# Performance work log

Measured on AMD Instinct MI355X. Metric: run time of the kernel, lower is better.

## Reference

```python
import jax, jax.numpy as jnp
import numpy as np

IGNORE_INDEX = -100
BETA = 0.1
VOCAB = 32000
HIDDEN = 4096
TWO_B = 8   # concatenated [chosen; rejected]
SEQ = 512


def setup_inputs() -> dict:
    key = jax.random.key(0)
    k1, k2, k3, k4, k5 = jax.random.split(key, 5)
    lin_weight = jax.random.normal(k1, (VOCAB, HIDDEN), dtype=jnp.float32) * 0.02
    _input = jax.random.normal(k2, (TWO_B, SEQ, HIDDEN), dtype=jnp.float32)
    target = jax.random.randint(k3, (TWO_B, SEQ), 0, VOCAB, dtype=jnp.int64)
    ref_chosen_logps = jax.random.normal(k4, (TWO_B // 2,), dtype=jnp.float32)
    ref_rejected_logps = jax.random.normal(k5, (TWO_B // 2,), dtype=jnp.float32)
    bias = jnp.zeros((VOCAB,), dtype=jnp.float32)
    return {"lin_weight": lin_weight, "_input": _input, "target": target,
            "ref_chosen_logps": ref_chosen_logps, "ref_rejected_logps": ref_rejected_logps,
            "bias": bias}


def reference(lin_weight, _input, target, ref_chosen_logps, ref_rejected_logps, bias):
    B2 = target.shape[0]
    len_chosen = B2 // 2
    # fused linear + log-softmax (materialized here; the kernel chunks this)
    logits = jnp.einsum("bth,vh->btv", _input, lin_weight) + bias  # [2B, T, V]
    logp = jax.nn.log_softmax(logits, axis=-1)
    mask = (target != IGNORE_INDEX)
    safe_tgt = jnp.where(mask, target, 0)
    per_tok = jnp.take_along_axis(logp, safe_tgt[..., None], axis=-1)[..., 0]
    per_tok = jnp.where(mask, per_tok, 0.0)                         # [2B, T]
    cnt = mask.sum(axis=-1).astype(per_tok.dtype)                   # tokens per sequence
    avg_logps = per_tok.sum(axis=-1) / cnt                          # average logp per sequence
    chosen_logps = avg_logps[:len_chosen]
    rejected_logps = avg_logps[len_chosen:]
    # NLL loss on chosen half, normalized by chosen non-ignored token count
    nll_loss = -per_tok[:len_chosen].sum() / mask[:len_chosen].sum().astype(per_tok.dtype)
    # DPO preference loss
    chosen_adv = chosen_logps - ref_chosen_logps
    rejected_adv = rejected_logps - ref_rejected_logps
    pref_logits = BETA * (chosen_adv - rejected_adv)
    pref_loss = -jnp.mean(jax.nn.log_sigmoid(pref_logits))
    return pref_loss + nll_loss
```

## Files before the change

### kernel.cpp

```cpp
#include <hip/hip_runtime.h>
#include <hip/hip_bf16.h>
#include <stdint.h>

#define M_TOK 4096
#define NV    32000
#define KH    4096
#define BM    128
#define BN    128
#define BK    64
#define NBLK  (NV / BN)
#define MBLK  (M_TOK / BM)
#define IGNORE_INDEX (-100)

typedef __bf16 bf16;
typedef bf16  bf16x8 __attribute__((ext_vector_type(8)));
typedef bf16  bf16x4 __attribute__((ext_vector_type(4)));
typedef float f32x4  __attribute__((ext_vector_type(4)));

__device__ __forceinline__ void async_copy16(const void* g, void* l) {
    __builtin_amdgcn_global_load_lds(
        (const __attribute__((address_space(1))) void*)g,
        (__attribute__((address_space(3))) void*)l, 16, 0, 0);
}

__global__ __launch_bounds__(256) void cvt_bf16_kernel(const float* __restrict__ src,
                                                       bf16* __restrict__ dst, int n4) {
    int i = blockIdx.x * blockDim.x + threadIdx.x;
    int stride = gridDim.x * blockDim.x;
    const float4* s4 = (const float4*)src;
    bf16x4* d4 = (bf16x4*)dst;
    for (; i < n4; i += stride) {
        float4 v = s4[i];
        bf16x4 o;
        o[0] = (bf16)v.x; o[1] = (bf16)v.y; o[2] = (bf16)v.z; o[3] = (bf16)v.w;
        d4[i] = o;
    }
}

__global__ __launch_bounds__(256) void tlogit_kernel(const float* __restrict__ inp,
                                                     const float* __restrict__ W,
                                                     const float* __restrict__ bias,
                                                     const int* __restrict__ target,
                                                     float* __restrict__ tlogit) {
    const int wave = threadIdx.x >> 6, lane = threadIdx.x & 63;
    const int t = blockIdx.x * 4 + wave;
    if (t >= M_TOK) return;
    int tg = target[t];
    int row = (tg == IGNORE_INDEX) ? 0 : tg;
    const float4* a4 = (const float4*)(inp + (long)t * KH);
    const float4* w4 = (const float4*)(W + (long)row * KH);
    float acc = 0.f;
#pragma unroll
    for (int i = 0; i < 16; i++) {
        float4 a = a4[i * 64 + lane];
        float4 w = w4[i * 64 + lane];
        acc += a.x * w.x + a.y * w.y + a.z * w.z + a.w * w.w;
    }
#pragma unroll
    for (int d = 1; d < 64; d <<= 1) acc += __shfl_xor(acc, d, 64);
    if (lane == 0) tlogit[t] = acc + bias[row];
}

template<bool PRECONV>
__global__ __launch_bounds__(256) void gemm_lse_kernel(const bf16* __restrict__ A,
                                                       const void* __restrict__ Wv,
                                                       const float* __restrict__ bias,
                                                       float* __restrict__ pm,
                                                       float* __restrict__ ps) {
    const int tid = threadIdx.x;
    const int wave = tid >> 6, lane = tid & 63;
    const int wm = wave & 1, wn = wave >> 1;
    const int bx = blockIdx.x;
    const int mblk = bx & 31;
    const int nblk = bx >> 5;
    const int m0 = mblk * BM, n0 = nblk * BN;

    __shared__ bf16 sA[BM * BK];
    __shared__ bf16 sB[BN * BK];
    __shared__ float red_m[2][BM];
    __shared__ float red_s[2][BM];

    f32x4 acc[4][4] = {};

    const int srow  = tid >> 3;
    const int slot  = tid & 7;
    const int chunk = slot ^ (srow & 7);
    const bf16* aptr = A + (long)(m0 + srow) * KH + chunk * 8;
    bf16* sA_dst = sA + tid * 8;
    bf16* sB_dst = sB + tid * 8;

    const bf16*  Wb = (const bf16*)Wv;
    const float* Wf = (const float*)Wv;
    const bf16*  bptr16 = Wb + (long)(n0 + srow) * KH + chunk * 8;
    const float* bptr32 = Wf + (long)(n0 + srow) * KH + chunk * 8;

    for (int k0 = 0; k0 < KH; k0 += BK) {
#pragma unroll
        for (int i = 0; i < 4; i++)
            async_copy16(aptr + (long)i * 32 * KH + k0, sA_dst + i * 2048);
        if (PRECONV) {
#pragma unroll
            for (int i = 0; i < 4; i++)
                async_copy16(bptr16 + (long)i * 32 * KH + k0, sB_dst + i * 2048);
        } else {
#pragma unroll
            for (int i = 0; i < 4; i++) {
                const float* wp = bptr32 + (long)i * 32 * KH + k0;
                float4 w0 = *(const float4*)(wp);
                float4 w1 = *(const float4*)(wp + 4);
                bf16x8 b;
                b[0] = (bf16)w0.x; b[1] = (bf16)w0.y; b[2] = (bf16)w0.z; b[3] = (bf16)w0.w;
                b[4] = (bf16)w1.x; b[5] = (bf16)w1.y; b[6] = (bf16)w1.z; b[7] = (bf16)w1.w;
                *(bf16x8*)(sB + (i * 32 + srow) * BK + slot * 8) = b;
            }
        }
        __syncthreads();
#pragma unroll
        for (int kk = 0; kk < BK; kk += 32) {
            bf16x8 af[4], bfr[4];
            const int rbase = wm * 64 + (lane & 15);
            const int cbase = wn * 64 + (lane & 15);
            const int c = (kk >> 3) + (lane >> 4);
            const int xoff = ((c ^ (lane & 7)) << 3);
#pragma unroll
            for (int t = 0; t < 4; t++)
                af[t] = *(const bf16x8*)(sA + (rbase + t * 16) * BK + xoff);
#pragma unroll
            for (int t = 0; t < 4; t++)
                bfr[t] = *(const bf16x8*)(sB + (cbase + t * 16) * BK + xoff);
#pragma unroll
            for (int mt = 0; mt < 4; mt++)
#pragma unroll
                for (int nt = 0; nt < 4; nt++)
                    acc[mt][nt] = __builtin_amdgcn_mfma_f32_16x16x32_bf16(
                        af[mt], bfr[nt], acc[mt][nt], 0, 0, 0);
        }
        __syncthreads();
    }

    float bv[4];
#pragma unroll
    for (int nt = 0; nt < 4; nt++)
        bv[nt] = bias[n0 + wn * 64 + nt * 16 + (lane & 15)];

#pragma unroll
    for (int mt = 0; mt < 4; mt++) {
        float rm[4], rs[4];
#pragma unroll
        for (int r = 0; r < 4; r++) {
            float v0 = acc[mt][0][r] + bv[0];
            float v1 = acc[mt][1][r] + bv[1];
            float v2 = acc[mt][2][r] + bv[2];
            float v3 = acc[mt][3][r] + bv[3];
            float mx = fmaxf(fmaxf(v0, v1), fmaxf(v2, v3));
#pragma unroll
            for (int d = 1; d < 16; d <<= 1) mx = fmaxf(mx, __shfl_xor(mx, d, 64));
            float s = __expf(v0 - mx) + __expf(v1 - mx) + __expf(v2 - mx) + __expf(v3 - mx);
#pragma unroll
            for (int d = 1; d < 16; d <<= 1) s += __shfl_xor(s, d, 64);
            rm[r] = mx; rs[r] = s;
        }
        if ((lane & 15) == 0) {
            int rl = wm * 64 + mt * 16 + (lane >> 4) * 4;
#pragma unroll
            for (int r = 0; r < 4; r++) {
                red_m[wn][rl + r] = rm[r];
                red_s[wn][rl + r] = rs[r];
            }
        }
    }
    __syncthreads();
    if (tid < BM) {
        float m0v = red_m[0][tid], s0v = red_s[0][tid];
        float m1v = red_m[1][tid], s1v = red_s[1][tid];
        float mm = fmaxf(m0v, m1v);
        float ss = s0v * __expf(m0v - mm) + s1v * __expf(m1v - mm);
        long idx = (long)nblk * M_TOK + m0 + tid;
        pm[idx] = mm;
        ps[idx] = ss;
    }
}

__global__ __launch_bounds__(256) void lse_combine_kernel(const float* __restrict__ pm,
                                                          const float* __restrict__ ps,
                                                          const float* __restrict__ tlogit,
                                                          const int* __restrict__ target,
                                                          float* __restrict__ per_tok) {
    int t = blockIdx.x * blockDim.x + threadIdx.x;
    if (t >= M_TOK) return;
    float m = -1e30f, s = 0.f;
    for (int j = 0; j < NBLK; j++) {
        float mj = pm[j * M_TOK + t];
        float sj = ps[j * M_TOK + t];
        if (mj > m) {
            s = s * expf(m - mj) + sj;
            m = mj;
        } else {
            s += sj * expf(mj - m);
        }
    }
    float lse = m + logf(s);
    int tg = target[t];
    per_tok[t] = (tg != IGNORE_INDEX) ? (tlogit[t] - lse) : 0.0f;
}

__global__ __launch_bounds__(512) void final_kernel(const float* __restrict__ per_tok,
                                                    const int* __restrict__ target,
                                                    const float* __restrict__ refc,
                                                    const float* __restrict__ refr,
                                                    float* __restrict__ out) {
    __shared__ float ssum[8];
    __shared__ float scnt[8];
    const int w = threadIdx.x >> 6, lane = threadIdx.x & 63;
    float sum = 0.f, cnt = 0.f;
#pragma unroll
    for (int i = 0; i < 8; i++) {
        int t = w * 512 + i * 64 + lane;
        sum += per_tok[t];
        cnt += (target[t] != IGNORE_INDEX) ? 1.f : 0.f;
    }
#pragma unroll
    for (int d = 1; d < 64; d <<= 1) {
        sum += __shfl_xor(sum, d, 64);
        cnt += __shfl_xor(cnt, d, 64);
    }
    if (lane == 0) { ssum[w] = sum; scnt[w] = cnt; }
    __syncthreads();
    if (threadIdx.x == 0) {
        float avg[8];
#pragma unroll
        for (int i = 0; i < 8; i++) avg[i] = ssum[i] / scnt[i];
        float nll_num = 0.f, nll_den = 0.f;
#pragma unroll
        for (int i = 0; i < 4; i++) { nll_num += ssum[i]; nll_den += scnt[i]; }
        float nll = -nll_num / nll_den;
        float pref = 0.f;
#pragma unroll
        for (int i = 0; i < 4; i++) {
            float x = 0.1f * ((avg[i] - refc[i]) - (avg[i + 4] - refr[i]));
            float ls = (x >= 0.f) ? -log1pf(expf(-x)) : (x - log1pf(expf(x)));
            pref += -ls;
        }
        pref *= 0.25f;
        out[0] = pref + nll;
    }
}

extern "C" void kernel_launch(void* const* d_in, const int* in_sizes, int n_in,
                              void* d_out, int out_size, void* d_ws, size_t ws_size,
                              hipStream_t stream) {
    const float* W    = (const float*)d_in[0];
    const float* inp  = (const float*)d_in[1];
    const int*   tgt  = (const int*)d_in[2];
    const float* refc = (const float*)d_in[3];
    const float* refr = (const float*)d_in[4];
    const float* bias = (const float*)d_in[5];
    float* out = (float*)d_out;

    char* ws = (char*)d_ws;
    size_t off = 0;
    bf16* A16 = (bf16*)(ws + off); off += (size_t)M_TOK * KH * sizeof(bf16);
    float* pm = (float*)(ws + off); off += (size_t)NBLK * M_TOK * sizeof(float);
    float* ps = (float*)(ws + off); off += (size_t)NBLK * M_TOK * sizeof(float);
    float* tl = (float*)(ws + off); off += (size_t)M_TOK * sizeof(float);
    float* ptk = (float*)(ws + off); off += (size_t)M_TOK * sizeof(float);
    bf16* W16 = (bf16*)(ws + off);
    size_t need = off + (size_t)NV * KH * sizeof(bf16);

    cvt_bf16_kernel<<<4096, 256, 0, stream>>>(inp, A16, (M_TOK * KH) / 4);
    tlogit_kernel<<<M_TOK / 4, 256, 0, stream>>>(inp, W, bias, tgt, tl);
    if (ws_size >= need) {
        cvt_bf16_kernel<<<16384, 256, 0, stream>>>(W, W16, (int)(((size_t)NV * KH) / 4));
        gemm_lse_kernel<true><<<MBLK * NBLK, 256, 0, stream>>>(A16, (const void*)W16, bias, pm, ps);
    } else {
        gemm_lse_kernel<false><<<MBLK * NBLK, 256, 0, stream>>>(A16, (const void*)W, bias, pm, ps);
    }
    lse_combine_kernel<<<(M_TOK + 255) / 256, 256, 0, stream>>>(pm, ps, tl, tgt, ptk);
    final_kernel<<<1, 512, 0, stream>>>(ptk, tgt, refc, refr, out);
}
```

Baseline: 2.127 ms.

## Add 256x256-tile double-buffered bf16 MFMA GEMM with fused log-sum-exp partials

Replaces the 128x128 GEMM+LSE kernel with a 512-thread, 256x256-tile kernel for the pre-converted-weight path. The new kernel double-buffers 128KB of LDS through async global-to-LDS copies into XOR-swizzled tiles. It interleaves quarter-tile MFMA groups with the next tile's loads, using explicit barriers, waitcnts and setprio. Blocks are remapped so neighbouring tiles land on the same XCD, and the combine kernel now takes the column-block count as a parameter. The aim is more data reuse per LDS byte and better overlap of loads with MFMA work. The cost is very high register and LDS use, so only one block fits per CU, and the hand-tuned wait counts are fragile.

Result: faster. 1.714 ms (-19.4%).

```diff
diff --git a/kernel.cpp b/kernel.cpp
--- a/kernel.cpp
+++ b/kernel.cpp
@@ -5,12 +5,14 @@
 #define M_TOK 4096
 #define NV    32000
 #define KH    4096
+#define KTILES 64
+#define IGNORE_INDEX (-100)
+
 #define BM    128
 #define BN    128
 #define BK    64
-#define NBLK  (NV / BN)
-#define MBLK  (M_TOK / BM)
-#define IGNORE_INDEX (-100)
+#define NBLK_OLD  (NV / BN)
+#define MBLK_OLD  (M_TOK / BM)
 
 typedef __bf16 bf16;
 typedef bf16  bf16x8 __attribute__((ext_vector_type(8)));
@@ -61,6 +63,180 @@
     if (lane == 0) tlogit[t] = acc + bias[row];
 }
 
+__global__ __launch_bounds__(512, 2) void gemm_lse256_kernel(
+    const bf16* __restrict__ A, const bf16* __restrict__ W16,
+    const float* __restrict__ bias, float* __restrict__ pm, float* __restrict__ ps)
+{
+    __shared__ __align__(16) char smem[131072];
+    const int tid = threadIdx.x;
+    const int lane = tid & 63;
+    const int wid = tid >> 6;
+    const int wm = wid >> 2, wn = wid & 3;
+
+    const int bx = blockIdx.x;
+    const int wg = (bx & 7) * 250 + (bx >> 3);
+    const int nblk = wg >> 4;
+    const int mblk = wg & 15;
+    const int m0 = mblk << 8;
+    const int n0 = nblk << 8;
+
+    const int srow = tid >> 3, slot = tid & 7;
+    const int chunk = slot ^ (srow & 7);
+    const bf16* aSrc = A   + (size_t)(m0 + srow) * KH + chunk * 8;
+    const bf16* bSrc = W16 + (size_t)(n0 + srow) * KH + chunk * 8;
+    char* dA0 = smem +      0 + tid * 16;
+    char* dB0 = smem +  32768 + tid * 16;
+    char* dA1 = smem +  65536 + tid * 16;
+    char* dB1 = smem +  98304 + tid * 16;
+
+#define STG_A(DST, h, tt) do { if ((tt) < KTILES) {                            \
+        const bf16* _s = aSrc + (size_t)(h) * 128 * KH + (size_t)(tt) * 64;    \
+        async_copy16(_s,                   (DST) + (h) * 16384);               \
+        async_copy16(_s + (size_t)64 * KH, (DST) + (h) * 16384 + 8192); } } while (0)
+#define STG_B(DST, h, tt) do { if ((tt) < KTILES) {                            \
+        const bf16* _s = bSrc + (size_t)(h) * 128 * KH + (size_t)(tt) * 64;    \
+        async_copy16(_s,                   (DST) + (h) * 16384);               \
+        async_copy16(_s + (size_t)64 * KH, (DST) + (h) * 16384 + 8192); } } while (0)
+
+    const int rA = wm * 128 + (lane & 15);
+    const int rB = wn * 64  + (lane & 15);
+    const int co0 = ((((lane >> 4) + 0) ^ (lane & 7)) << 3);
+    const int co1 = ((((lane >> 4) + 4) ^ (lane & 7)) << 3);
+
+    const bf16* sA[2] = { (const bf16*)(smem),         (const bf16*)(smem + 65536) };
+    const bf16* sB[2] = { (const bf16*)(smem + 32768), (const bf16*)(smem + 98304) };
+
+    f32x4 acc[8][4] = {};
+    bf16x8 regA[8], regB0[4], regB1[4];
+
+#define MFMA_Q(MB, NB, BR)                                                      \
+    _Pragma("unroll")                                                           \
+    for (int mt = 0; mt < 4; ++mt)                                              \
+        _Pragma("unroll")                                                       \
+        for (int nt = 0; nt < 2; ++nt)                                          \
+            _Pragma("unroll")                                                   \
+            for (int ks = 0; ks < 2; ++ks)                                      \
+                acc[(MB) + mt][(NB) + nt] = __builtin_amdgcn_mfma_f32_16x16x32_bf16( \
+                    regA[mt * 2 + ks], BR[nt * 2 + ks], acc[(MB) + mt][(NB) + nt], 0, 0, 0);
+
+#define TILE_BODY(b, t, DA_O, DB_C, DA_C) do {                                  \
+                                                      \
+    _Pragma("unroll") for (int mt = 0; mt < 4; ++mt) {                          \
+        regA[mt * 2]     = *(const bf16x8*)(sA[b] + (rA + mt * 16) * 64 + co0); \
+        regA[mt * 2 + 1] = *(const bf16x8*)(sA[b] + (rA + mt * 16) * 64 + co1); } \
+    _Pragma("unroll") for (int nt = 0; nt < 2; ++nt) {                          \
+        regB0[nt * 2]     = *(const bf16x8*)(sB[b] + (rB + nt * 16) * 64 + co0); \
+        regB0[nt * 2 + 1] = *(const bf16x8*)(sB[b] + (rB + nt * 16) * 64 + co1); } \
+    STG_A(DA_O, 1, (t) + 1);                                                    \
+    __builtin_amdgcn_s_barrier();                                               \
+    asm volatile("s_waitcnt lgkmcnt(0)" ::: "memory");                          \
+    __builtin_amdgcn_sched_barrier(0);                                          \
+    __builtin_amdgcn_s_setprio(1);                                              \
+    MFMA_Q(0, 0, regB0)                                                         \
+    __builtin_amdgcn_s_setprio(0);                                              \
+    __builtin_amdgcn_s_barrier();                                               \
+                                                      \
+    _Pragma("unroll") for (int nt = 0; nt < 2; ++nt) {                          \
+        regB1[nt * 2]     = *(const bf16x8*)(sB[b] + (rB + (nt + 2) * 16) * 64 + co0); \
+        regB1[nt * 2 + 1] = *(const bf16x8*)(sB[b] + (rB + (nt + 2) * 16) * 64 + co1); } \
+    __builtin_amdgcn_s_barrier();                                               \
+    asm volatile("s_waitcnt lgkmcnt(0)" ::: "memory");                          \
+    __builtin_amdgcn_sched_barrier(0);                                          \
+    __builtin_amdgcn_s_setprio(1);                                              \
+    MFMA_Q(0, 2, regB1)                                                         \
+    __builtin_amdgcn_s_setprio(0);                                              \
+    __builtin_amdgcn_s_barrier();                                               \
+                                                      \
+    _Pragma("unroll") for (int mt = 0; mt < 4; ++mt) {                          \
+        regA[mt * 2]     = *(const bf16x8*)(sA[b] + (rA + (mt + 4) * 16) * 64 + co0); \
+        regA[mt * 2 + 1] = *(const bf16x8*)(sA[b] + (rA + (mt + 4) * 16) * 64 + co1); } \
+    STG_B(DB_C, 0, (t) + 2);                                                    \
+    __builtin_amdgcn_s_barrier();                                               \
+    asm volatile("s_waitcnt lgkmcnt(0)" ::: "memory");                          \
+    __builtin_amdgcn_sched_barrier(0);                                          \
+    __builtin_amdgcn_s_setprio(1);                                              \
+    MFMA_Q(4, 2, regB1)                                                         \
+    __builtin_amdgcn_s_setprio(0);                                              \
+    __builtin_amdgcn_s_barrier();                                               \
+                                                      \
+    STG_B(DB_C, 1, (t) + 2);                                                    \
+    STG_A(DA_C, 0, (t) + 2);                                                    \
+    __builtin_amdgcn_s_barrier();                                               \
+    __builtin_amdgcn_s_setprio(1);                                              \
+    MFMA_Q(4, 0, regB0)                                                         \
+    __builtin_amdgcn_s_setprio(0);                                              \
+    if ((t) + 2 < KTILES) { asm volatile("s_waitcnt vmcnt(6)" ::: "memory"); }  \
+    else                  { asm volatile("s_waitcnt vmcnt(0)" ::: "memory"); }  \
+    __builtin_amdgcn_s_barrier();                                               \
+} while (0)
+
+    STG_A(dA0, 0, 0); STG_A(dA0, 1, 0);
+    STG_B(dB0, 0, 0); STG_B(dB0, 1, 0);
+    STG_B(dB1, 0, 1); STG_B(dB1, 1, 1);
+    STG_A(dA1, 0, 1);
+    asm volatile("s_waitcnt vmcnt(6)" ::: "memory");
+    __builtin_amdgcn_s_barrier();
+
+#pragma unroll 1
+    for (int t = 0; t < KTILES; t += 2) {
+        TILE_BODY(0, t,     dA1, dB0, dA0);
+        TILE_BODY(1, t + 1, dA0, dB1, dA1);
+    }
+
+    float bv[4];
+#pragma unroll
+    for (int nt = 0; nt < 4; ++nt)
+        bv[nt] = bias[n0 + wn * 64 + nt * 16 + (lane & 15)];
+
+    float (*red_m)[256] = (float (*)[256])(smem);
+    float (*red_s)[256] = (float (*)[256])(smem + 4096);
+
+#pragma unroll
+    for (int mt = 0; mt < 8; ++mt) {
+        float rm[4], rs[4];
+#pragma unroll
+        for (int r = 0; r < 4; ++r) {
+            float v0 = acc[mt][0][r] + bv[0];
+            float v1 = acc[mt][1][r] + bv[1];
+            float v2 = acc[mt][2][r] + bv[2];
+            float v3 = acc[mt][3][r] + bv[3];
+            float mx = fmaxf(fmaxf(v0, v1), fmaxf(v2, v3));
+#pragma unroll
+            for (int d = 1; d < 16; d <<= 1) mx = fmaxf(mx, __shfl_xor(mx, d, 64));
+            float s = __expf(v0 - mx) + __expf(v1 - mx) + __expf(v2 - mx) + __expf(v3 - mx);
+#pragma unroll
+            for (int d = 1; d < 16; d <<= 1) s += __shfl_xor(s, d, 64);
+            rm[r] = mx; rs[r] = s;
+        }
+        if ((lane & 15) == 0) {
+            int rl = wm * 128 + mt * 16 + (lane >> 4) * 4;
+#pragma unroll
+            for (int r = 0; r < 4; ++r) {
+                red_m[wn][rl + r] = rm[r];
+                red_s[wn][rl + r] = rs[r];
+            }
+        }
+    }
+    __syncthreads();
+    if (tid < 256) {
+        float mm = red_m[0][tid], ss = red_s[0][tid];
+#pragma unroll
+        for (int j = 1; j < 4; ++j) {
+            float mj = red_m[j][tid], sj = red_s[j][tid];
+            float m2 = fmaxf(mm, mj);
+            ss = ss * __expf(mm - m2) + sj * __expf(mj - m2);
+            mm = m2;
+        }
+        size_t idx = (size_t)nblk * M_TOK + m0 + tid;
+        pm[idx] = mm;
+        ps[idx] = ss;
+    }
+#undef TILE_BODY
+#undef MFMA_Q
+#undef STG_A
+#undef STG_B
+}
+
 template<bool PRECONV>
 __global__ __launch_bounds__(256) void gemm_lse_kernel(const bf16* __restrict__ A,
                                                        const void* __restrict__ Wv,
@@ -185,11 +361,12 @@
                                                           const float* __restrict__ ps,
                                                           const float* __restrict__ tlogit,
                                                           const int* __restrict__ target,
-                                                          float* __restrict__ per_tok) {
+                                                          float* __restrict__ per_tok,
+                                                          int nblkN) {
     int t = blockIdx.x * blockDim.x + threadIdx.x;
     if (t >= M_TOK) return;
     float m = -1e30f, s = 0.f;
-    for (int j = 0; j < NBLK; j++) {
+    for (int j = 0; j < nblkN; j++) {
         float mj = pm[j * M_TOK + t];
         float sj = ps[j * M_TOK + t];
         if (mj > m) {
@@ -260,8 +437,8 @@
     char* ws = (char*)d_ws;
     size_t off = 0;
     bf16* A16 = (bf16*)(ws + off); off += (size_t)M_TOK * KH * sizeof(bf16);
-    float* pm = (float*)(ws + off); off += (size_t)NBLK * M_TOK * sizeof(float);
-    float* ps = (float*)(ws + off); off += (size_t)NBLK * M_TOK * sizeof(float);
+    float* pm = (float*)(ws + off); off += (size_t)NBLK_OLD * M_TOK * sizeof(float);
+    float* ps = (float*)(ws + off); off += (size_t)NBLK_OLD * M_TOK * sizeof(float);
     float* tl = (float*)(ws + off); off += (size_t)M_TOK * sizeof(float);
     float* ptk = (float*)(ws + off); off += (size_t)M_TOK * sizeof(float);
     bf16* W16 = (bf16*)(ws + off);
@@ -271,10 +448,11 @@
     tlogit_kernel<<<M_TOK / 4, 256, 0, stream>>>(inp, W, bias, tgt, tl);
     if (ws_size >= need) {
         cvt_bf16_kernel<<<16384, 256, 0, stream>>>(W, W16, (int)(((size_t)NV * KH) / 4));
-        gemm_lse_kernel<true><<<MBLK * NBLK, 256, 0, stream>>>(A16, (const void*)W16, bias, pm, ps);
+        gemm_lse256_kernel<<<16 * 125, 512, 0, stream>>>(A16, W16, bias, pm, ps);
+        lse_combine_kernel<<<(M_TOK + 255) / 256, 256, 0, stream>>>(pm, ps, tl, tgt, ptk, 125);
     } else {
-        gemm_lse_kernel<false><<<MBLK * NBLK, 256, 0, stream>>>(A16, (const void*)W, bias, pm, ps);
-    }
-    lse_combine_kernel<<<(M_TOK + 255) / 256, 256, 0, stream>>>(pm, ps, tl, tgt, ptk);
+        gemm_lse_kernel<false><<<MBLK_OLD * NBLK_OLD, 256, 0, stream>>>(A16, (const void*)W, bias, pm, ps);
+        lse_combine_kernel<<<(M_TOK + 255) / 256, 256, 0, stream>>>(pm, ps, tl, tgt, ptk, NBLK_OLD);
+    }
     final_kernel<<<1, 512, 0, stream>>>(ptk, tgt, refc, refr, out);
 }
```
